# Kernel optimization log

Measured on AMD Instinct MI355X. Metric: run time of the kernel, lower is better.

The kernel has to match this reference:

```python
import jax, jax.numpy as jnp
import numpy as np

D_MODEL = 2048
N_HEADS = 16
D_HEAD = D_MODEL // N_HEADS  # 128
RANK = 32


def _orthogonal(key, rows, cols, dtype=jnp.float32):
    # mimic torch orthogonal init via QR
    a = jax.random.normal(key, (max(rows, cols), min(rows, cols)), dtype=jnp.float32)
    q, r = jnp.linalg.qr(a)
    q = q * jnp.sign(jnp.diagonal(r))
    if rows < cols:
        q = q.T
    return q.astype(dtype)


def setup_inputs() -> dict:
    key = jax.random.key(0)
    ks = jax.random.split(key, 8)
    B, T = 2, 2048
    x = jax.random.normal(ks[0], (B, T, D_MODEL), dtype=jnp.float32)
    s = 1.0 / np.sqrt(D_MODEL)
    Wq = jax.random.uniform(ks[1], (D_MODEL, D_MODEL), minval=-s, maxval=s, dtype=jnp.float32)
    Wk = jax.random.uniform(ks[2], (D_MODEL, D_MODEL), minval=-s, maxval=s, dtype=jnp.float32)
    Wv = jax.random.uniform(ks[3], (D_MODEL, D_MODEL), minval=-s, maxval=s, dtype=jnp.float32)
    Wo = jax.random.uniform(ks[4], (D_MODEL, D_MODEL), minval=-s, maxval=s, dtype=jnp.float32)
    # vein projector: project d_head -> rank, reconstruct rank -> d_head (orthogonal init)
    Wdown = _orthogonal(ks[5], D_HEAD, RANK)   # [d_head, r]
    Wup = _orthogonal(ks[6], RANK, D_HEAD)     # [r, d_head]
    return {"x": x, "Wq": Wq, "Wk": Wk, "Wv": Wv, "Wo": Wo, "Wdown": Wdown, "Wup": Wup}


def reference(x, Wq, Wk, Wv, Wo, Wdown, Wup):
    B, T, D = x.shape
    H, dh, r = N_HEADS, D_HEAD, RANK
    scale = 1.0 / np.sqrt(r)

    def heads(y):  # [B,T,D] -> [B,H,T,dh]
        return y.reshape(B, T, H, dh).transpose(0, 2, 1, 3)

    q = heads(x @ Wq.T)
    k = heads(x @ Wk.T)
    v = heads(x @ Wv.T)

    # project into vein (rank) space: [B,H,T,r]
    q_r = jnp.einsum('bhtd,dr->bhtr', q, Wdown)
    k_r = jnp.einsum('bhtd,dr->bhtr', k, Wdown)
    v_r = jnp.einsum('bhtd,dr->bhtr', v, Wdown)

    scores = jnp.einsum('bhqr,bhkr->bhqk', q_r, k_r) * scale  # [B,H,T,T]
    attn = jax.nn.softmax(scores, axis=-1)
    y_r = jnp.einsum('bhqk,bhkr->bhqr', attn, v_r)            # [B,H,T,r]
    y = jnp.einsum('bhtr,rd->bhtd', y_r, Wup)                  # reconstruct [B,H,T,dh]
    y = y.transpose(0, 2, 1, 3).reshape(B, T, D)
    out = y @ Wo.T
    return out
```

## Files before the change

kernel.cpp:

```cpp
#include <hip/hip_runtime.h>
#include <cstdint>
#include <cstddef>

typedef __bf16 bf16;
typedef __attribute__((ext_vector_type(8))) __bf16 bf16x8;
typedef __attribute__((ext_vector_type(4))) __bf16 bf16x4;
typedef __attribute__((ext_vector_type(2))) __bf16 bf16x2;
typedef __attribute__((ext_vector_type(4))) float f32x4;
typedef unsigned int u32;

#define D_MODEL 2048
#define QSCALE  0.17677669529663687f

__device__ inline void async_load16(const void* gp, void* lp) {
  __builtin_amdgcn_global_load_lds(
      (const __attribute__((address_space(1))) u32*)gp,
      (__attribute__((address_space(3))) u32*)lp, 16, 0, 0);
}

__global__ __launch_bounds__(256) void cvt_k(const float* __restrict__ x,
                                             bf16* __restrict__ xb) {
  const int i = (blockIdx.x * 256 + threadIdx.x) * 8;
  float4 a = *(const float4*)(x + i);
  float4 b = *(const float4*)(x + i + 4);
  bf16x8 o;
  o[0] = (bf16)a.x; o[1] = (bf16)a.y; o[2] = (bf16)a.z; o[3] = (bf16)a.w;
  o[4] = (bf16)b.x; o[5] = (bf16)b.y; o[6] = (bf16)b.z; o[7] = (bf16)b.w;
  *(bf16x8*)(xb + i) = o;
}

__global__ __launch_bounds__(256) void fold_qkv_k(
    const float* __restrict__ Wq, const float* __restrict__ Wk,
    const float* __restrict__ Wv, const float* __restrict__ Wdown,
    bf16* __restrict__ EffT) {
  __shared__ float wd[128][32];
  const int t = threadIdx.x;
  for (int i = t; i < 128 * 32; i += 256)
    ((float*)wd)[i] = Wdown[i];
  __syncthreads();
  const int mh = blockIdx.x;
  const float* W = (mh < 16) ? Wq : ((mh < 32) ? Wk : Wv);
  const int hrow = (mh & 15) * 128;
  const int d = blockIdx.y * 128 + (t & 127);
  const int rh = (t >> 7) * 16;
  float acc[16];
#pragma unroll
  for (int j = 0; j < 16; ++j) acc[j] = 0.f;
#pragma unroll 4
  for (int k = 0; k < 128; ++k) {
    float w = W[(size_t)(hrow + k) * D_MODEL + d];
    const float* wr = &wd[k][rh];
#pragma unroll
    for (int j = 0; j < 16; ++j) acc[j] += w * wr[j];
  }
  bf16* outp = EffT + (size_t)(mh * 32 + rh) * D_MODEL + d;
#pragma unroll
  for (int j = 0; j < 16; ++j) outp[(size_t)j * D_MODEL] = (bf16)acc[j];
}

__global__ __launch_bounds__(256) void fold_o_k(
    const bf16* __restrict__ Wob, const float* __restrict__ Wup,
    bf16* __restrict__ WoEffT) {
  __shared__ __align__(16) bf16 As_[128 * 128];
  __shared__ __align__(16) bf16 Bs_[32 * 128];
  const int t = threadIdx.x, wave = t >> 6, lane = t & 63;
  const int quad = lane >> 4, lc = lane & 15;
  const int d0 = blockIdx.x * 128, h = blockIdx.y;
#pragma unroll
  for (int a = 0; a < 8; ++a) {
    int r0 = wave * 32 + a * 4;
    int row = r0 + (lane >> 4);
    int g = (lane & 15) ^ (row & 15);
    async_load16(Wob + (size_t)(d0 + row) * 2048 + h * 128 + g * 8,
                 As_ + r0 * 128);
  }
  {
    int row = t >> 3;
    int c0 = (t & 7) * 2;
    const float* src = Wup + row * 128 + c0 * 8;
    float4 f0 = ((const float4*)src)[0], f1 = ((const float4*)src)[1];
    float4 f2 = ((const float4*)src)[2], f3 = ((const float4*)src)[3];
    bf16x8 b0, b1;
    b0[0] = (bf16)f0.x; b0[1] = (bf16)f0.y; b0[2] = (bf16)f0.z; b0[3] = (bf16)f0.w;
    b0[4] = (bf16)f1.x; b0[5] = (bf16)f1.y; b0[6] = (bf16)f1.z; b0[7] = (bf16)f1.w;
    b1[0] = (bf16)f2.x; b1[1] = (bf16)f2.y; b1[2] = (bf16)f2.z; b1[3] = (bf16)f2.w;
    b1[4] = (bf16)f3.x; b1[5] = (bf16)f3.y; b1[6] = (bf16)f3.z; b1[7] = (bf16)f3.w;
    *(bf16x8*)(Bs_ + row * 128 + ((c0 ^ (row & 15)) * 8)) = b0;
    *(bf16x8*)(Bs_ + row * 128 + (((c0 + 1) ^ (row & 15)) * 8)) = b1;
  }
  __syncthreads();
  f32x4 acc[2][2] = {};
  const int wm = wave * 32;
#pragma unroll
  for (int kc = 0; kc < 4; ++kc) {
    bf16x8 af[2], bfr[2];
#pragma unroll
    for (int mi = 0; mi < 2; ++mi) {
      int m = wm + mi * 16 + lc;
      af[mi] = *(const bf16x8*)(As_ + m * 128 + (((kc * 4 + quad) ^ (m & 15)) * 8));
    }
#pragma unroll
    for (int ni = 0; ni < 2; ++ni) {
      int n = ni * 16 + lc;
      bfr[ni] = *(const bf16x8*)(Bs_ + n * 128 + (((kc * 4 + quad) ^ (n & 15)) * 8));
    }
#pragma unroll
    for (int mi = 0; mi < 2; ++mi)
#pragma unroll
      for (int ni = 0; ni < 2; ++ni)
        acc[mi][ni] = __builtin_amdgcn_mfma_f32_16x16x32_bf16(
            af[mi], bfr[ni], acc[mi][ni], 0, 0, 0);
  }
#pragma unroll
  for (int mi = 0; mi < 2; ++mi)
#pragma unroll
    for (int ni = 0; ni < 2; ++ni)
#pragma unroll
      for (int reg = 0; reg < 4; ++reg)
        WoEffT[(size_t)(d0 + wm + mi * 16 + quad * 4 + reg) * 512 + h * 32 +
               ni * 16 + lc] = (bf16)acc[mi][ni][reg];
}

template <int EPI>
__global__ __launch_bounds__(256) void gemm_bt_k(
    const bf16* __restrict__ A, const bf16* __restrict__ Bt,
    void* __restrict__ Cv, int M, int N, int K) {
  __shared__ __align__(16) bf16 As[2][128 * 64];
  __shared__ __align__(16) bf16 Bs[2][128 * 64];
  const int t = threadIdx.x, wave = t >> 6, lane = t & 63;
  const int quad = lane >> 4, lc = lane & 15;
  const size_t m0 = (size_t)blockIdx.x * 128;
  const size_t n0 = (size_t)blockIdx.y * 128;
  const int wm = (wave >> 1) * 64, wn = (wave & 1) * 64;
  const int sr = lane >> 3, ss = lane & 7;
  const bf16* Aga[4]; const bf16* Bga[4]; int Loff[4];
#pragma unroll
  for (int a = 0; a < 4; ++a) {
    int row = wave * 32 + a * 8 + sr;
    Aga[a] = A + (m0 + row) * (size_t)K + (ss ^ (row & 7)) * 8;
    Bga[a] = Bt + (n0 + row) * (size_t)K + (ss ^ (row & 7)) * 8;
    Loff[a] = (wave * 32 + a * 8) * 64;
  }
  f32x4 acc[4][4] = {};
  const int NIT = K >> 6;
#pragma unroll
  for (int a = 0; a < 4; ++a) {
    async_load16(Aga[a], &As[0][Loff[a]]);
    async_load16(Bga[a], &Bs[0][Loff[a]]);
  }
  __syncthreads();
  for (int it = 0; it < NIT; ++it) {
    const int cur = it & 1;
    if (it + 1 < NIT) {
      const int k0 = (it + 1) * 64;
#pragma unroll
      for (int a = 0; a < 4; ++a) {
        async_load16(Aga[a] + k0, &As[1 - cur][Loff[a]]);
        async_load16(Bga[a] + k0, &Bs[1 - cur][Loff[a]]);
      }
    }
    const bf16* Asb = As[cur];
    const bf16* Bsb = Bs[cur];
#pragma unroll
    for (int kc = 0; kc < 2; ++kc) {
      bf16x8 af[4], bfr[4];
#pragma unroll
      for (int mi = 0; mi < 4; ++mi) {
        int m = wm + mi * 16 + lc;
        af[mi] = *(const bf16x8*)(Asb + m * 64 + (((kc * 4 + quad) ^ (m & 7)) * 8));
      }
#pragma unroll
      for (int ni = 0; ni < 4; ++ni) {
        int n = wn + ni * 16 + lc;
        bfr[ni] = *(const bf16x8*)(Bsb + n * 64 + (((kc * 4 + quad) ^ (n & 7)) * 8));
      }
#pragma unroll
      for (int mi = 0; mi < 4; ++mi)
#pragma unroll
        for (int ni = 0; ni < 4; ++ni)
          acc[mi][ni] = __builtin_amdgcn_mfma_f32_16x16x32_bf16(
              af[mi], bfr[ni], acc[mi][ni], 0, 0, 0);
    }
    __syncthreads();
  }

  if (EPI == 0) {
    float* C = (float*)Cv;
#pragma unroll
    for (int mi = 0; mi < 4; ++mi)
#pragma unroll
      for (int ni = 0; ni < 4; ++ni) {
        size_t row = m0 + wm + mi * 16 + quad * 4;
        size_t col = n0 + wn + ni * 16 + lc;
#pragma unroll
        for (int reg = 0; reg < 4; ++reg)
          C[(row + reg) * (size_t)N + col] = acc[mi][ni][reg];
      }
  } else {
    bf16* C = (bf16*)Cv;
#pragma unroll
    for (int mi = 0; mi < 4; ++mi)
#pragma unroll
      for (int ni = 0; ni < 4; ++ni) {
        int n = (int)n0 + wn + ni * 16 + lc;
        int mat = n >> 9, hh = (n >> 5) & 15, r = n & 31;
        float sc = (mat == 0) ? QSCALE : 1.0f;
        int trow = (int)m0 + wm + mi * 16 + quad * 4;
#pragma unroll
        for (int reg = 0; reg < 4; ++reg) {
          int tr = trow + reg;
          int b = tr >> 11, tl = tr & 2047;
          size_t off = ((((size_t)(b * 16 + hh)) * 3 + mat) * 2048 + tl) * 32 + r;
          C[off] = (bf16)(acc[mi][ni][reg] * sc);
        }
      }
  }
}

__global__ __launch_bounds__(256) void attn_k(const bf16* __restrict__ QKVr,
                                              bf16* __restrict__ Yr) {
  const int bh = blockIdx.x, qb = blockIdx.y;
  const size_t base = (size_t)bh * 3 * 2048 * 32;
  const bf16* Q  = QKVr + base;
  const bf16* Kr = Q + 2048 * 32;
  const bf16* Vr = Kr + 2048 * 32;
  __shared__ __align__(16) bf16 Ks[2][128 * 32];
  __shared__ __align__(16) bf16 Vt[2][32 * 128];
  __shared__ __align__(16) bf16 Ps[4 * 32 * 128];
  const int t = threadIdx.x, wave = t >> 6, lane = t & 63;
  const int quad = lane >> 4, lc = lane & 15;
  const int qbase = qb * 128 + wave * 32;
  const bf16x8 qf0 = *(const bf16x8*)(Q + (size_t)(qbase + lc) * 32 + quad * 8);
  const bf16x8 qf1 = *(const bf16x8*)(Q + (size_t)(qbase + 16 + lc) * 32 + quad * 8);
  f32x4 o00 = {}, o01 = {}, o10 = {}, o11 = {};
  float ls0 = 0.f, ls1 = 0.f;
  const int krow = wave * 16 + (lane >> 2);
  const bf16* Kg = Kr + (size_t)krow * 32 + ((lane & 3) ^ ((krow >> 1) & 3)) * 8;
  const int va_ = t >> 2;
  const int vrs = (t & 3) * 8;
  bf16* pw = Ps + wave * 32 * 128;

  async_load16(Kg, &Ks[0][wave * 16 * 32]);
  async_load16(Kg + (size_t)64 * 32, &Ks[0][(64 + wave * 16) * 32]);
  {
    bf16x8 va = *(const bf16x8*)(Vr + (size_t)(2 * va_) * 32 + vrs);
    bf16x8 vb = *(const bf16x8*)(Vr + (size_t)(2 * va_ + 1) * 32 + vrs);
#pragma unroll
    for (int j = 0; j < 8; ++j) {
      int r = vrs + j;
      bf16x2 p = {va[j], vb[j]};
      *(bf16x2*)(Vt[0] + r * 128 + (((va_ >> 2) ^ (r & 15)) * 8) + (va_ & 3) * 2) = p;
    }
  }
  __syncthreads();

  for (int it = 0; it < 16; ++it) {
    const int kt = it * 128, cur = it & 1;
    bf16x8 na, nb;
    if (it < 15) {
      async_load16(Kg + (size_t)(kt + 128) * 32, &Ks[1 - cur][wave * 16 * 32]);
      async_load16(Kg + (size_t)(kt + 192) * 32, &Ks[1 - cur][(64 + wave * 16) * 32]);
      na = *(const bf16x8*)(Vr + (size_t)(kt + 128 + 2 * va_) * 32 + vrs);
      nb = *(const bf16x8*)(Vr + (size_t)(kt + 128 + 2 * va_ + 1) * 32 + vrs);
    }
    const bf16* ksb = Ks[cur];
#pragma unroll
    for (int ni = 0; ni < 8; ++ni) {
      int n = ni * 16 + lc;
      bf16x8 kf = *(const bf16x8*)(ksb + n * 32 + ((quad ^ ((n >> 1) & 3)) * 8));
      f32x4 z = {0.f, 0.f, 0.f, 0.f};
      f32x4 s0 = __builtin_amdgcn_mfma_f32_16x16x32_bf16(kf, qf0, z, 0, 0, 0);
      f32x4 s1 = __builtin_amdgcn_mfma_f32_16x16x32_bf16(kf, qf1, z, 0, 0, 0);
      bf16x4 p0, p1;
#pragma unroll
      for (int reg = 0; reg < 4; ++reg) {
        float e0 = __expf(s0[reg]); ls0 += e0; p0[reg] = (bf16)e0;
        float e1 = __expf(s1[reg]); ls1 += e1; p1[reg] = (bf16)e1;
      }
      int off = (((2 * ni + (quad >> 1)) ^ lc) * 8) + (quad & 1) * 4;
      *(bf16x4*)(pw + lc * 128 + off) = p0;
      *(bf16x4*)(pw + (16 + lc) * 128 + off) = p1;
    }
    const bf16* vtb = Vt[cur];
#pragma unroll
    for (int kc = 0; kc < 4; ++kc) {
      int co = ((kc * 4 + quad) ^ lc) * 8;
      bf16x8 pf0 = *(const bf16x8*)(pw + lc * 128 + co);
      bf16x8 pf1 = *(const bf16x8*)(pw + (16 + lc) * 128 + co);
      bf16x8 v0 = *(const bf16x8*)(vtb + lc * 128 + co);
      bf16x8 v1 = *(const bf16x8*)(vtb + (16 + lc) * 128 + co);
      o00 = __builtin_amdgcn_mfma_f32_16x16x32_bf16(pf0, v0, o00, 0, 0, 0);
      o01 = __builtin_amdgcn_mfma_f32_16x16x32_bf16(pf0, v1, o01, 0, 0, 0);
      o10 = __builtin_amdgcn_mfma_f32_16x16x32_bf16(pf1, v0, o10, 0, 0, 0);
      o11 = __builtin_amdgcn_mfma_f32_16x16x32_bf16(pf1, v1, o11, 0, 0, 0);
    }
    if (it < 15) {
#pragma unroll
      for (int j = 0; j < 8; ++j) {
        int r = vrs + j;
        bf16x2 p = {na[j], nb[j]};
        *(bf16x2*)(Vt[1 - cur] + r * 128 + (((va_ >> 2) ^ (r & 15)) * 8) + (va_ & 3) * 2) = p;
      }
    }
    __syncthreads();
  }
  ls0 += __shfl_xor(ls0, 16); ls0 += __shfl_xor(ls0, 32);
  ls1 += __shfl_xor(ls1, 16); ls1 += __shfl_xor(ls1, 32);
  const int b = bh >> 4, h = bh & 15;
#pragma unroll
  for (int reg = 0; reg < 4; ++reg) {
    float i0 = 1.0f / __shfl(ls0, quad * 4 + reg);
    float i1 = 1.0f / __shfl(ls1, quad * 4 + reg);
    size_t r0 = (size_t)b * 2048 + qbase + quad * 4 + reg;
    size_t r1 = r0 + 16;
    Yr[r0 * 512 + h * 32 + lc]      = (bf16)(o00[reg] * i0);
    Yr[r0 * 512 + h * 32 + 16 + lc] = (bf16)(o01[reg] * i0);
    Yr[r1 * 512 + h * 32 + lc]      = (bf16)(o10[reg] * i1);
    Yr[r1 * 512 + h * 32 + 16 + lc] = (bf16)(o11[reg] * i1);
  }
}

extern "C" void kernel_launch(void* const* d_in, const int* in_sizes, int n_in,
                              void* d_out, int out_size, void* d_ws, size_t ws_size,
                              hipStream_t stream) {
  const float* x     = (const float*)d_in[0];
  const float* Wq    = (const float*)d_in[1];
  const float* Wk    = (const float*)d_in[2];
  const float* Wv    = (const float*)d_in[3];
  const float* Wo    = (const float*)d_in[4];
  const float* Wdown = (const float*)d_in[5];
  const float* Wup   = (const float*)d_in[6];
  float* out = (float*)d_out;

  char* ws = (char*)d_ws;
  bf16* EffT   = (bf16*)(ws);
  bf16* WoEffT = (bf16*)(ws + 6291456);
  bf16* QKVr   = (bf16*)(ws + 8388608);
  bf16* Wob    = (bf16*)(ws + 8388608);
  bf16* Yrb    = (bf16*)(ws + 20971520);
  bf16* xb     = (bf16*)(ws + 25165824);

  cvt_k<<<dim3(4096), dim3(256), 0, stream>>>(x, xb);
  cvt_k<<<dim3(2048), dim3(256), 0, stream>>>(Wo, Wob);
  fold_qkv_k<<<dim3(48, 16), dim3(256), 0, stream>>>(Wq, Wk, Wv, Wdown, EffT);
  fold_o_k<<<dim3(16, 16), dim3(256), 0, stream>>>(Wob, Wup, WoEffT);
  gemm_bt_k<1><<<dim3(32, 12), dim3(256), 0, stream>>>(xb, EffT, QKVr,
                                                       4096, 1536, 2048);
  attn_k<<<dim3(32, 16), dim3(256), 0, stream>>>(QKVr, Yrb);
  gemm_bt_k<0><<<dim3(32, 16), dim3(256), 0, stream>>>(Yrb, WoEffT, out,
                                                       4096, 2048, 512);
}
```

Before: 254.0 us.

## Pre-transpose V in projection epilogue, async-load V, compute rowsums via MFMA

The QKV projection epilogue now writes V in a pre-transposed, XOR-swizzled per-128-key tile layout. The attention kernel can then fetch V with direct global-to-LDS async loads instead of register loads followed by a scalar transpose into shared memory. The softmax denominator is now an extra MFMA against a ones vector instead of a per-lane float sum with shuffles, and the log2(e) factor is folded into the Q scale so exp2f can replace __expf. s_setprio hints are wrapped around the MFMA sections. In exchange, the projection epilogue uses a scattered store pattern for V, and the row sums are accumulated from bf16-rounded probabilities.

```diff
diff --git a/kernel.cpp b/kernel.cpp
--- a/kernel.cpp
+++ b/kernel.cpp
@@ -10,7 +10,8 @@
 typedef unsigned int u32;
 
 #define D_MODEL 2048
-#define QSCALE  0.17677669529663687f
+#define QSCALE      0.17677669529663687f
+#define QSCALE_L2E  (0.17677669529663687f * 1.4426950408889634f)
 
 __device__ inline void async_load16(const void* gp, void* lp) {
   __builtin_amdgcn_global_load_lds(
@@ -204,13 +205,21 @@
       for (int ni = 0; ni < 4; ++ni) {
         int n = (int)n0 + wn + ni * 16 + lc;
         int mat = n >> 9, hh = (n >> 5) & 15, r = n & 31;
-        float sc = (mat == 0) ? QSCALE : 1.0f;
+        float sc = (mat == 0) ? QSCALE_L2E : 1.0f;
         int trow = (int)m0 + wm + mi * 16 + quad * 4;
 #pragma unroll
         for (int reg = 0; reg < 4; ++reg) {
           int tr = trow + reg;
           int b = tr >> 11, tl = tr & 2047;
-          size_t off = ((((size_t)(b * 16 + hh)) * 3 + mat) * 2048 + tl) * 32 + r;
+          size_t off;
+          if (mat == 2) {
+            int tile = tl >> 7, kin = tl & 127;
+            off = ((size_t)(b * 16 + hh) * 3 + 2) * 65536 +
+                  (size_t)tile * 4096 + r * 128 +
+                  (((kin >> 3) ^ (r & 15)) << 3) + (kin & 7);
+          } else {
+            off = (((size_t)(b * 16 + hh) * 3 + mat) * 2048 + tl) * 32 + r;
+          }
           C[off] = (bf16)(acc[mi][ni][reg] * sc);
         }
       }
@@ -233,35 +242,28 @@
   const bf16x8 qf0 = *(const bf16x8*)(Q + (size_t)(qbase + lc) * 32 + quad * 8);
   const bf16x8 qf1 = *(const bf16x8*)(Q + (size_t)(qbase + 16 + lc) * 32 + quad * 8);
   f32x4 o00 = {}, o01 = {}, o10 = {}, o11 = {};
-  float ls0 = 0.f, ls1 = 0.f;
+  f32x4 os0 = {}, os1 = {};
+  bf16x8 ones;
+#pragma unroll
+  for (int j = 0; j < 8; ++j) ones[j] = (bf16)1.0f;
   const int krow = wave * 16 + (lane >> 2);
   const bf16* Kg = Kr + (size_t)krow * 32 + ((lane & 3) ^ ((krow >> 1) & 3)) * 8;
-  const int va_ = t >> 2;
-  const int vrs = (t & 3) * 8;
   bf16* pw = Ps + wave * 32 * 128;
 
   async_load16(Kg, &Ks[0][wave * 16 * 32]);
   async_load16(Kg + (size_t)64 * 32, &Ks[0][(64 + wave * 16) * 32]);
-  {
-    bf16x8 va = *(const bf16x8*)(Vr + (size_t)(2 * va_) * 32 + vrs);
-    bf16x8 vb = *(const bf16x8*)(Vr + (size_t)(2 * va_ + 1) * 32 + vrs);
-#pragma unroll
-    for (int j = 0; j < 8; ++j) {
-      int r = vrs + j;
-      bf16x2 p = {va[j], vb[j]};
-      *(bf16x2*)(Vt[0] + r * 128 + (((va_ >> 2) ^ (r & 15)) * 8) + (va_ & 3) * 2) = p;
-    }
-  }
+  async_load16(Vr + (wave * 2) * 512 + lane * 8, &Vt[0][(wave * 2) * 512]);
+  async_load16(Vr + (wave * 2 + 1) * 512 + lane * 8, &Vt[0][(wave * 2 + 1) * 512]);
   __syncthreads();
 
   for (int it = 0; it < 16; ++it) {
     const int kt = it * 128, cur = it & 1;
-    bf16x8 na, nb;
     if (it < 15) {
       async_load16(Kg + (size_t)(kt + 128) * 32, &Ks[1 - cur][wave * 16 * 32]);
       async_load16(Kg + (size_t)(kt + 192) * 32, &Ks[1 - cur][(64 + wave * 16) * 32]);
-      na = *(const bf16x8*)(Vr + (size_t)(kt + 128 + 2 * va_) * 32 + vrs);
-      nb = *(const bf16x8*)(Vr + (size_t)(kt + 128 + 2 * va_ + 1) * 32 + vrs);
+      const bf16* vg = Vr + (size_t)(it + 1) * 4096;
+      async_load16(vg + (wave * 2) * 512 + lane * 8, &Vt[1 - cur][(wave * 2) * 512]);
+      async_load16(vg + (wave * 2 + 1) * 512 + lane * 8, &Vt[1 - cur][(wave * 2 + 1) * 512]);
     }
     const bf16* ksb = Ks[cur];
 #pragma unroll
@@ -269,19 +271,22 @@
       int n = ni * 16 + lc;
       bf16x8 kf = *(const bf16x8*)(ksb + n * 32 + ((quad ^ ((n >> 1) & 3)) * 8));
       f32x4 z = {0.f, 0.f, 0.f, 0.f};
+      __builtin_amdgcn_s_setprio(1);
       f32x4 s0 = __builtin_amdgcn_mfma_f32_16x16x32_bf16(kf, qf0, z, 0, 0, 0);
       f32x4 s1 = __builtin_amdgcn_mfma_f32_16x16x32_bf16(kf, qf1, z, 0, 0, 0);
+      __builtin_amdgcn_s_setprio(0);
       bf16x4 p0, p1;
 #pragma unroll
       for (int reg = 0; reg < 4; ++reg) {
-        float e0 = __expf(s0[reg]); ls0 += e0; p0[reg] = (bf16)e0;
-        float e1 = __expf(s1[reg]); ls1 += e1; p1[reg] = (bf16)e1;
+        p0[reg] = (bf16)exp2f(s0[reg]);
+        p1[reg] = (bf16)exp2f(s1[reg]);
       }
       int off = (((2 * ni + (quad >> 1)) ^ lc) * 8) + (quad & 1) * 4;
       *(bf16x4*)(pw + lc * 128 + off) = p0;
       *(bf16x4*)(pw + (16 + lc) * 128 + off) = p1;
     }
     const bf16* vtb = Vt[cur];
+    __builtin_amdgcn_s_setprio(1);
 #pragma unroll
     for (int kc = 0; kc < 4; ++kc) {
       int co = ((kc * 4 + quad) ^ lc) * 8;
@@ -293,24 +298,17 @@
       o01 = __builtin_amdgcn_mfma_f32_16x16x32_bf16(pf0, v1, o01, 0, 0, 0);
       o10 = __builtin_amdgcn_mfma_f32_16x16x32_bf16(pf1, v0, o10, 0, 0, 0);
       o11 = __builtin_amdgcn_mfma_f32_16x16x32_bf16(pf1, v1, o11, 0, 0, 0);
-    }
-    if (it < 15) {
-#pragma unroll
-      for (int j = 0; j < 8; ++j) {
-        int r = vrs + j;
-        bf16x2 p = {na[j], nb[j]};
-        *(bf16x2*)(Vt[1 - cur] + r * 128 + (((va_ >> 2) ^ (r & 15)) * 8) + (va_ & 3) * 2) = p;
-      }
-    }
+      os0 = __builtin_amdgcn_mfma_f32_16x16x32_bf16(pf0, ones, os0, 0, 0, 0);
+      os1 = __builtin_amdgcn_mfma_f32_16x16x32_bf16(pf1, ones, os1, 0, 0, 0);
+    }
+    __builtin_amdgcn_s_setprio(0);
     __syncthreads();
   }
-  ls0 += __shfl_xor(ls0, 16); ls0 += __shfl_xor(ls0, 32);
-  ls1 += __shfl_xor(ls1, 16); ls1 += __shfl_xor(ls1, 32);
   const int b = bh >> 4, h = bh & 15;
 #pragma unroll
   for (int reg = 0; reg < 4; ++reg) {
-    float i0 = 1.0f / __shfl(ls0, quad * 4 + reg);
-    float i1 = 1.0f / __shfl(ls1, quad * 4 + reg);
+    float i0 = 1.0f / os0[reg];
+    float i1 = 1.0f / os1[reg];
     size_t r0 = (size_t)b * 2048 + qbase + quad * 4 + reg;
     size_t r1 = r0 + 16;
     Yr[r0 * 512 + h * 32 + lc]      = (bf16)(o00[reg] * i0);
```

Measured after the change: 265.7 us. 1.05x slower.
